# Kernel tuning notes

Measured on AMD Instinct MI355X. Metric: run time of the kernel, lower is better.

Reference implementation:

```python
import jax, jax.numpy as jnp
import numpy as np

B, P, H, D = 32, 512, 512, 512

def setup_inputs() -> dict:
    key = jax.random.key(0)
    k1, k2, k3, k4 = jax.random.split(key, 4)
    px = jax.random.normal(k1, (B, P, D), dtype=jnp.float32)
    hx = jax.random.normal(k2, (B, H, D), dtype=jnp.float32)
    p_mask = jax.random.randint(k3, (B, P), 0, 2) == 1  # True = padded
    h_mask = jax.random.randint(k4, (B, H), 0, 2) == 1
    return {"px": px, "hx": hx, "p_mask": p_mask, "h_mask": h_mask}

def reference(px, hx, p_mask, h_mask):
    # shared (unscaled) score matrix: [B, P, H]
    e = jnp.einsum('bpd,bhd->bph', px, hx)
    neg_inf = jnp.float32(-jnp.inf)
    h_bias = jnp.where(h_mask, neg_inf, 0.0).astype(e.dtype)  # [B, H]
    p_bias = jnp.where(p_mask, neg_inf, 0.0).astype(e.dtype)  # [B, P]
    # softmax over hypothesis axis -> attend px to hx
    weight_b = jax.nn.softmax(e + h_bias[:, None, :], axis=2)  # [B, P, H]
    px_hat = jnp.einsum('bph,bhd->bpd', weight_b, hx)
    # softmax over premise axis -> attend hx to px
    weight_a = jax.nn.softmax(e + p_bias[:, :, None], axis=1)  # [B, P, H]
    hx_hat = jnp.einsum('bph,bpd->bhd', weight_a, px)
    m_p = jnp.concatenate([px, px_hat, px - px_hat, px * px_hat], axis=-1)
    m_h = jnp.concatenate([hx, hx_hat, hx - hx_hat, hx * hx_hat], axis=-1)
    return (m_p, m_h)
```

## Files before the change

### kernel.cpp

```cpp
#include <hip/hip_runtime.h>
#include <math.h>

#define NB 32
#define NN 512
#define ROWC 2048ull

typedef __attribute__((ext_vector_type(8))) short bf16x8;
typedef __attribute__((ext_vector_type(4))) float f32x4;

__device__ __forceinline__ unsigned int fbits(float f) {
  union { float f; unsigned int u; } v; v.f = f; return v.u;
}
__device__ __forceinline__ float bcast(unsigned int u) {
  union { unsigned int u; float f; } v; v.u = u; return v.f;
}
__device__ __forceinline__ unsigned int bf16_rne(float f) {
  unsigned int b = fbits(f);
  return (b + 0x7FFFu + ((b >> 16) & 1u)) >> 16;
}

__device__ __forceinline__ int frag_byte(int blk, int lane, int khalf) {
  int base = ((((khalf << 3) + blk) << 6) + lane) << 4;
  int swz = (blk ^ (lane >> 4) ^ (khalf << 2)) & 7;
  return base ^ (swz << 4);
}

__global__ __launch_bounds__(256) void gemm_e_stats(
    const float* __restrict__ px, const float* __restrict__ hx,
    const int* __restrict__ p_mask, const int* __restrict__ h_mask,
    float* __restrict__ e,
    float* __restrict__ rpm, float* __restrict__ rps,
    float* __restrict__ cpm, float* __restrict__ cps) {
  __shared__ union {
    struct { char Ah[16384]; char Al[16384]; char Bh[16384]; char Bl[16384]; } s;
    float ep[64][132];
  } u;
  __shared__ int pmk[128], hmk[128];
  __shared__ float st_m[2][128], st_s[2][128], sc_m[2][128], sc_s[2][128];
  const int b = blockIdx.z;
  const float* A = px + (size_t)b * NN * NN;
  const float* B = hx + (size_t)b * NN * NN;
  float* C = e + (size_t)b * NN * NN;
  const int row0 = blockIdx.y * 128, col0 = blockIdx.x * 128;
  const int t = threadIdx.x;
  const int l = t & 63, w = t >> 6;
  const int wr = w >> 1, wc = w & 1;
  const int g = l >> 4, li = l & 15;

  if (t < 128) pmk[t] = p_mask[(size_t)b * NN + row0 + t];
  else hmk[t - 128] = h_mask[(size_t)b * NN + col0 + (t - 128)];

  f32x4 acc[4][4];
#pragma unroll
  for (int i = 0; i < 4; ++i)
#pragma unroll
    for (int j = 0; j < 4; ++j)
#pragma unroll
      for (int r = 0; r < 4; ++r) acc[i][j][r] = 0.f;

  for (int k0 = 0; k0 < NN; k0 += 64) {
    float4 fa[8], fb[8];
#pragma unroll
    for (int i = 0; i < 8; ++i) {
      int idx = i * 256 + t;
      fa[i] = *(const float4*)&A[(size_t)(row0 + (idx >> 4)) * NN + k0 + ((idx & 15) << 2)];
    }
#pragma unroll
    for (int i = 0; i < 8; ++i) {
      int idx = i * 256 + t;
      fb[i] = *(const float4*)&B[(size_t)(col0 + (idx >> 4)) * NN + k0 + ((idx & 15) << 2)];
    }
#pragma unroll
    for (int i = 0; i < 8; ++i) {
      int idx = i * 256 + t;
      int r = idx >> 4, k = (idx & 15) << 2;
      float4 f = fa[i];
      unsigned int b0 = fbits(f.x), b1 = fbits(f.y), b2 = fbits(f.z), b3 = fbits(f.w);
      unsigned int h01 = (b0 >> 16) | (b1 & 0xFFFF0000u);
      unsigned int h23 = (b2 >> 16) | (b3 & 0xFFFF0000u);
      float r0 = f.x - bcast(b0 & 0xFFFF0000u);
      float r1 = f.y - bcast(b1 & 0xFFFF0000u);
      float r2 = f.z - bcast(b2 & 0xFFFF0000u);
      float r3 = f.w - bcast(b3 & 0xFFFF0000u);
      unsigned int l01 = (fbits(r0) >> 16) | (fbits(r1) & 0xFFFF0000u);
      unsigned int l23 = (fbits(r2) >> 16) | (fbits(r3) & 0xFFFF0000u);
      int khalf = k >> 5, k8 = (k >> 3) & 3, j = k & 7;
      int byte = frag_byte(r >> 4, (r & 15) + (k8 << 4), khalf) + (j << 1);
      *(uint2*)&u.s.Ah[byte] = make_uint2(h01, h23);
      *(uint2*)&u.s.Al[byte] = make_uint2(l01, l23);
    }
#pragma unroll
    for (int i = 0; i < 8; ++i) {
      int idx = i * 256 + t;
      int r = idx >> 4, k = (idx & 15) << 2;
      float4 f = fb[i];
      unsigned int b0 = fbits(f.x), b1 = fbits(f.y), b2 = fbits(f.z), b3 = fbits(f.w);
      unsigned int h01 = (b0 >> 16) | (b1 & 0xFFFF0000u);
      unsigned int h23 = (b2 >> 16) | (b3 & 0xFFFF0000u);
      float r0 = f.x - bcast(b0 & 0xFFFF0000u);
      float r1 = f.y - bcast(b1 & 0xFFFF0000u);
      float r2 = f.z - bcast(b2 & 0xFFFF0000u);
      float r3 = f.w - bcast(b3 & 0xFFFF0000u);
      unsigned int l01 = (fbits(r0) >> 16) | (fbits(r1) & 0xFFFF0000u);
      unsigned int l23 = (fbits(r2) >> 16) | (fbits(r3) & 0xFFFF0000u);
      int khalf = k >> 5, k8 = (k >> 3) & 3, j = k & 7;
      int byte = frag_byte(r >> 4, (r & 15) + (k8 << 4), khalf) + (j << 1);
      *(uint2*)&u.s.Bh[byte] = make_uint2(h01, h23);
      *(uint2*)&u.s.Bl[byte] = make_uint2(l01, l23);
    }
    __syncthreads();
#pragma unroll
    for (int kh = 0; kh < 2; ++kh) {
      bf16x8 ah[4], al[4], bh[4], bl[4];
#pragma unroll
      for (int i = 0; i < 4; ++i) {
        int ab = frag_byte(wr * 4 + i, l, kh);
        ah[i] = *(const bf16x8*)&u.s.Ah[ab];
        al[i] = *(const bf16x8*)&u.s.Al[ab];
        int bb = frag_byte(wc * 4 + i, l, kh);
        bh[i] = *(const bf16x8*)&u.s.Bh[bb];
        bl[i] = *(const bf16x8*)&u.s.Bl[bb];
      }
#pragma unroll
      for (int i = 0; i < 4; ++i)
#pragma unroll
        for (int j = 0; j < 4; ++j) {
          acc[i][j] = __builtin_amdgcn_mfma_f32_16x16x32_bf16(ah[i], bh[j], acc[i][j], 0, 0, 0);
          acc[i][j] = __builtin_amdgcn_mfma_f32_16x16x32_bf16(ah[i], bl[j], acc[i][j], 0, 0, 0);
          acc[i][j] = __builtin_amdgcn_mfma_f32_16x16x32_bf16(al[i], bh[j], acc[i][j], 0, 0, 0);
        }
    }
    __syncthreads();
  }

#pragma unroll
  for (int i = 0; i < 4; ++i)
#pragma unroll
    for (int r = 0; r < 4; ++r) {
      float v[4];
      float m = -INFINITY;
#pragma unroll
      for (int j = 0; j < 4; ++j) {
        v[j] = hmk[wc * 64 + j * 16 + li] ? -INFINITY : acc[i][j][r];
        m = fmaxf(m, v[j]);
      }
#pragma unroll
      for (int o = 1; o < 16; o <<= 1) m = fmaxf(m, __shfl_xor(m, o));
      float s = 0.f;
#pragma unroll
      for (int j = 0; j < 4; ++j) s += (v[j] == -INFINITY) ? 0.f : __expf(v[j] - m);
#pragma unroll
      for (int o = 1; o < 16; o <<= 1) s += __shfl_xor(s, o);
      if (li == 0) {
        st_m[wc][wr * 64 + i * 16 + g * 4 + r] = m;
        st_s[wc][wr * 64 + i * 16 + g * 4 + r] = s;
      }
    }

#pragma unroll
  for (int j = 0; j < 4; ++j) {
    float v[16];
    float m = -INFINITY;
#pragma unroll
    for (int i = 0; i < 4; ++i)
#pragma unroll
      for (int r = 0; r < 4; ++r) {
        float x = pmk[wr * 64 + i * 16 + g * 4 + r] ? -INFINITY : acc[i][j][r];
        v[i * 4 + r] = x;
        m = fmaxf(m, x);
      }
    m = fmaxf(m, __shfl_xor(m, 16));
    m = fmaxf(m, __shfl_xor(m, 32));
    float s = 0.f;
#pragma unroll
    for (int q = 0; q < 16; ++q) s += (v[q] == -INFINITY) ? 0.f : __expf(v[q] - m);
    s += __shfl_xor(s, 16);
    s += __shfl_xor(s, 32);
    if (g == 0) {
      sc_m[wr][wc * 64 + j * 16 + li] = m;
      sc_s[wr][wc * 64 + j * 16 + li] = s;
    }
  }
  __syncthreads();

  if (t < 128) {
    float m0 = st_m[0][t], m1 = st_m[1][t];
    float s0 = st_s[0][t], s1 = st_s[1][t];
    float m = fmaxf(m0, m1);
    float s = 0.f;
    if (s0 > 0.f) s += s0 * __expf(m0 - m);
    if (s1 > 0.f) s += s1 * __expf(m1 - m);
    rpm[((size_t)b * 4 + blockIdx.x) * NN + row0 + t] = m;
    rps[((size_t)b * 4 + blockIdx.x) * NN + row0 + t] = s;
  } else {
    int c = t - 128;
    float m0 = sc_m[0][c], m1 = sc_m[1][c];
    float s0 = sc_s[0][c], s1 = sc_s[1][c];
    float m = fmaxf(m0, m1);
    float s = 0.f;
    if (s0 > 0.f) s += s0 * __expf(m0 - m);
    if (s1 > 0.f) s += s1 * __expf(m1 - m);
    cpm[((size_t)b * 4 + blockIdx.y) * NN + col0 + c] = m;
    cps[((size_t)b * 4 + blockIdx.y) * NN + col0 + c] = s;
  }

#pragma unroll
  for (int pass = 0; pass < 2; ++pass) {
    __syncthreads();
    if (wr == pass) {
#pragma unroll
      for (int i = 0; i < 4; ++i)
#pragma unroll
        for (int j = 0; j < 4; ++j)
#pragma unroll
          for (int r = 0; r < 4; ++r)
            u.ep[i * 16 + g * 4 + r][wc * 64 + j * 16 + li] = acc[i][j][r];
    }
    __syncthreads();
#pragma unroll
    for (int i = 0; i < 8; ++i) {
      int idx = i * 256 + t;
      int r = idx >> 5, c4 = idx & 31;
      int grow = row0 + pass * 64 + r;
      float4 v = *(const float4*)&u.ep[r][c4 * 4];
      *(float4*)&C[(size_t)grow * NN + col0 + c4 * 4] = v;
    }
  }
}

__global__ __launch_bounds__(512) void merge_stats(
    const float* __restrict__ rpm, const float* __restrict__ rps,
    const float* __restrict__ cpm, const float* __restrict__ cps,
    float* __restrict__ rmax, float* __restrict__ rinv,
    float* __restrict__ cmax, float* __restrict__ cinv) {
  const int b = blockIdx.x;
  const int t = threadIdx.x;
  const float* pm = blockIdx.y == 0 ? rpm : cpm;
  const float* ps = blockIdx.y == 0 ? rps : cps;
  float* fm = blockIdx.y == 0 ? rmax : cmax;
  float* fi = blockIdx.y == 0 ? rinv : cinv;
  float mj[4], sj[4];
  float m = -INFINITY;
#pragma unroll
  for (int j = 0; j < 4; ++j) {
    mj[j] = pm[((size_t)b * 4 + j) * NN + t];
    sj[j] = ps[((size_t)b * 4 + j) * NN + t];
    m = fmaxf(m, mj[j]);
  }
  float s = 0.f;
#pragma unroll
  for (int j = 0; j < 4; ++j)
    if (sj[j] > 0.f) s += sj[j] * __expf(mj[j] - m);
  fm[(size_t)b * NN + t] = m;
  fi[(size_t)b * NN + t] = 1.0f / s;
}

__global__ __launch_bounds__(256) void gemm_wp(
    const float* __restrict__ E, const float* __restrict__ hxg,
    const float* __restrict__ pxg, const int* __restrict__ h_mask,
    const float* __restrict__ rmax, const float* __restrict__ rinv,
    float* __restrict__ outg) {
  __shared__ union {
    struct { char A[16384]; char B[16384]; } s;
    float ep[64][132];
  } u;
  const int b = blockIdx.z;
  const float* Eb = E + (size_t)b * NN * NN;
  const float* B = hxg + (size_t)b * NN * NN;
  const float* X = pxg + (size_t)b * NN * NN;
  const int* hm = h_mask + (size_t)b * NN;
  const float* rmx = rmax + (size_t)b * NN;
  const float* rin = rinv + (size_t)b * NN;
  float* out = outg + (size_t)b * NN * ROWC;
  const int row0 = blockIdx.y * 128, col0 = blockIdx.x * 128;
  const int t = threadIdx.x;
  const int l = t & 63, w = t >> 6;
  const int wr = w >> 1, wc = w & 1;

  float rmv[8];
#pragma unroll
  for (int i = 0; i < 8; ++i) rmv[i] = rmx[row0 + ((i * 256 + t) >> 4)];

  f32x4 acc[4][4];
#pragma unroll
  for (int i = 0; i < 4; ++i)
#pragma unroll
    for (int j = 0; j < 4; ++j)
#pragma unroll
      for (int r = 0; r < 4; ++r) acc[i][j][r] = 0.f;

  for (int k0 = 0; k0 < NN; k0 += 64) {
#pragma unroll
    for (int i = 0; i < 8; ++i) {
      int idx = i * 256 + t;
      int r = idx >> 4, c4 = idx & 15, k = c4 << 2;
      float4 f = *(const float4*)&Eb[(size_t)(row0 + r) * NN + k0 + k];
      int4 m4 = *(const int4*)&hm[k0 + k];
      float w0 = m4.x ? 0.f : __expf(f.x - rmv[i]);
      float w1 = m4.y ? 0.f : __expf(f.y - rmv[i]);
      float w2 = m4.z ? 0.f : __expf(f.z - rmv[i]);
      float w3 = m4.w ? 0.f : __expf(f.w - rmv[i]);
      unsigned int p01 = bf16_rne(w0) | (bf16_rne(w1) << 16);
      unsigned int p23 = bf16_rne(w2) | (bf16_rne(w3) << 16);
      int khalf = k >> 5, k8 = (k >> 3) & 3, j = k & 7;
      int byte = frag_byte(r >> 4, (r & 15) + (k8 << 4), khalf) + (j << 1);
      *(uint2*)&u.s.A[byte] = make_uint2(p01, p23);
    }
#pragma unroll
    for (int i = 0; i < 4; ++i) {
      int idx = i * 256 + t;
      int kp = idx >> 5, nq = idx & 31;
      int k = kp << 1, n = nq << 2;
      const float* p0 = &B[(size_t)(k0 + k) * NN + col0 + n];
      float4 f0 = *(const float4*)p0;
      float4 f1 = *(const float4*)(p0 + NN);
      int khalf = k >> 5, k8 = (k >> 3) & 3, j = k & 7;
      float fa0[4] = {f0.x, f0.y, f0.z, f0.w};
      float fa1[4] = {f1.x, f1.y, f1.z, f1.w};
#pragma unroll
      for (int c = 0; c < 4; ++c) {
        unsigned int pk = bf16_rne(fa0[c]) | (bf16_rne(fa1[c]) << 16);
        int nn2 = n + c;
        int byte = frag_byte(nn2 >> 4, (nn2 & 15) + (k8 << 4), khalf) + (j << 1);
        *(unsigned int*)&u.s.B[byte] = pk;
      }
    }
    __syncthreads();
#pragma unroll
    for (int kh = 0; kh < 2; ++kh) {
      bf16x8 av[4], bv[4];
#pragma unroll
      for (int i = 0; i < 4; ++i) {
        av[i] = *(const bf16x8*)&u.s.A[frag_byte(wr * 4 + i, l, kh)];
        bv[i] = *(const bf16x8*)&u.s.B[frag_byte(wc * 4 + i, l, kh)];
      }
#pragma unroll
      for (int i = 0; i < 4; ++i)
#pragma unroll
        for (int j = 0; j < 4; ++j)
          acc[i][j] = __builtin_amdgcn_mfma_f32_16x16x32_bf16(av[i], bv[j], acc[i][j], 0, 0, 0);
    }
    __syncthreads();
  }

  const int g = l >> 4, li = l & 15;
#pragma unroll
  for (int pass = 0; pass < 2; ++pass) {
    if (wr == pass) {
#pragma unroll
      for (int i = 0; i < 4; ++i)
#pragma unroll
        for (int j = 0; j < 4; ++j)
#pragma unroll
          for (int r = 0; r < 4; ++r)
            u.ep[i * 16 + g * 4 + r][wc * 64 + j * 16 + li] = acc[i][j][r];
    }
    __syncthreads();
#pragma unroll
    for (int i = 0; i < 8; ++i) {
      int idx = i * 256 + t;
      int r = idx >> 5, c4 = idx & 31;
      int grow = row0 + pass * 64 + r;
      float ri = rin[grow];
      float4 ph = *(const float4*)&u.ep[r][c4 * 4];
      ph.x *= ri; ph.y *= ri; ph.z *= ri; ph.w *= ri;
      float4 xv = *(const float4*)&X[(size_t)grow * NN + col0 + c4 * 4];
      size_t base = (size_t)grow * ROWC + col0 + c4 * 4;
      *(float4*)&out[base] = xv;
      *(float4*)&out[base + 512] = ph;
      float4 df = {xv.x - ph.x, xv.y - ph.y, xv.z - ph.z, xv.w - ph.w};
      *(float4*)&out[base + 1024] = df;
      float4 pr = {xv.x * ph.x, xv.y * ph.y, xv.z * ph.z, xv.w * ph.w};
      *(float4*)&out[base + 1536] = pr;
    }
    __syncthreads();
  }
}

__global__ __launch_bounds__(256) void gemm_wh(
    const float* __restrict__ E, const float* __restrict__ pxg,
    const float* __restrict__ hxg, const int* __restrict__ p_mask,
    const float* __restrict__ cmax, const float* __restrict__ cinv,
    float* __restrict__ outg) {
  __shared__ union {
    struct { char A[16384]; char B[16384]; } s;
    float ep[64][132];
  } u;
  const int b = blockIdx.z;
  const float* Eb = E + (size_t)b * NN * NN;
  const float* B = pxg + (size_t)b * NN * NN;
  const float* X = hxg + (size_t)b * NN * NN;
  const int* pmsk = p_mask + (size_t)b * NN;
  const float* cmx = cmax + (size_t)b * NN;
  const float* cin = cinv + (size_t)b * NN;
  float* out = outg + (size_t)b * NN * ROWC;
  const int row0 = blockIdx.y * 128, col0 = blockIdx.x * 128;
  const int t = threadIdx.x;
  const int l = t & 63, w = t >> 6;
  const int wr = w >> 1, wc = w & 1;

  float4 cmv[4];
#pragma unroll
  for (int i = 0; i < 4; ++i) {
    int idx = i * 256 + t;
    int n = (idx & 31) << 2;
    cmv[i] = *(const float4*)&cmx[row0 + n];
  }

  f32x4 acc[4][4];
#pragma unroll
  for (int i = 0; i < 4; ++i)
#pragma unroll
    for (int j = 0; j < 4; ++j)
#pragma unroll
      for (int r = 0; r < 4; ++r) acc[i][j][r] = 0.f;

  for (int k0 = 0; k0 < NN; k0 += 64) {
#pragma unroll
    for (int i = 0; i < 4; ++i) {
      int idx = i * 256 + t;
      int kp = idx >> 5, nq = idx & 31;
      int k = kp << 1, n = nq << 2;
      const float* p0 = &Eb[(size_t)(k0 + k) * NN + row0 + n];
      float4 f0 = *(const float4*)p0;
      float4 f1 = *(const float4*)(p0 + NN);
      int pm0 = pmsk[k0 + k], pm1 = pmsk[k0 + k + 1];
      float fa0[4] = {f0.x, f0.y, f0.z, f0.w};
      float fa1[4] = {f1.x, f1.y, f1.z, f1.w};
      float cma[4] = {cmv[i].x, cmv[i].y, cmv[i].z, cmv[i].w};
      int khalf = k >> 5, k8 = (k >> 3) & 3, j = k & 7;
#pragma unroll
      for (int c = 0; c < 4; ++c) {
        float w0 = pm0 ? 0.f : __expf(fa0[c] - cma[c]);
        float w1 = pm1 ? 0.f : __expf(fa1[c] - cma[c]);
        unsigned int pk = bf16_rne(w0) | (bf16_rne(w1) << 16);
        int nn2 = n + c;
        int byte = frag_byte(nn2 >> 4, (nn2 & 15) + (k8 << 4), khalf) + (j << 1);
        *(unsigned int*)&u.s.A[byte] = pk;
      }
    }
#pragma unroll
    for (int i = 0; i < 4; ++i) {
      int idx = i * 256 + t;
      int kp = idx >> 5, nq = idx & 31;
      int k = kp << 1, n = nq << 2;
      const float* p0 = &B[(size_t)(k0 + k) * NN + col0 + n];
      float4 f0 = *(const float4*)p0;
      float4 f1 = *(const float4*)(p0 + NN);
      int khalf = k >> 5, k8 = (k >> 3) & 3, j = k & 7;
      float fa0[4] = {f0.x, f0.y, f0.z, f0.w};
      float fa1[4] = {f1.x, f1.y, f1.z, f1.w};
#pragma unroll
      for (int c = 0; c < 4; ++c) {
        unsigned int pk = bf16_rne(fa0[c]) | (bf16_rne(fa1[c]) << 16);
        int nn2 = n + c;
        int byte = frag_byte(nn2 >> 4, (nn2 & 15) + (k8 << 4), khalf) + (j << 1);
        *(unsigned int*)&u.s.B[byte] = pk;
      }
    }
    __syncthreads();
#pragma unroll
    for (int kh = 0; kh < 2; ++kh) {
      bf16x8 av[4], bv[4];
#pragma unroll
      for (int i = 0; i < 4; ++i) {
        av[i] = *(const bf16x8*)&u.s.A[frag_byte(wr * 4 + i, l, kh)];
        bv[i] = *(const bf16x8*)&u.s.B[frag_byte(wc * 4 + i, l, kh)];
      }
#pragma unroll
      for (int i = 0; i < 4; ++i)
#pragma unroll
        for (int j = 0; j < 4; ++j)
          acc[i][j] = __builtin_amdgcn_mfma_f32_16x16x32_bf16(av[i], bv[j], acc[i][j], 0, 0, 0);
    }
    __syncthreads();
  }

  const int g = l >> 4, li = l & 15;
#pragma unroll
  for (int pass = 0; pass < 2; ++pass) {
    if (wr == pass) {
#pragma unroll
      for (int i = 0; i < 4; ++i)
#pragma unroll
        for (int j = 0; j < 4; ++j)
#pragma unroll
          for (int r = 0; r < 4; ++r)
            u.ep[i * 16 + g * 4 + r][wc * 64 + j * 16 + li] = acc[i][j][r];
    }
    __syncthreads();
#pragma unroll
    for (int i = 0; i < 8; ++i) {
      int idx = i * 256 + t;
      int r = idx >> 5, c4 = idx & 31;
      int grow = row0 + pass * 64 + r;
      float ci = cin[grow];
      float4 hh = *(const float4*)&u.ep[r][c4 * 4];
      hh.x *= ci; hh.y *= ci; hh.z *= ci; hh.w *= ci;
      float4 xv = *(const float4*)&X[(size_t)grow * NN + col0 + c4 * 4];
      size_t base = (size_t)grow * ROWC + col0 + c4 * 4;
      *(float4*)&out[base] = xv;
      *(float4*)&out[base + 512] = hh;
      float4 df = {xv.x - hh.x, xv.y - hh.y, xv.z - hh.z, xv.w - hh.w};
      *(float4*)&out[base + 1024] = df;
      float4 pr = {xv.x * hh.x, xv.y * hh.y, xv.z * hh.z, xv.w * hh.w};
      *(float4*)&out[base + 1536] = pr;
    }
    __syncthreads();
  }
}

extern "C" void kernel_launch(void* const* d_in, const int* in_sizes, int n_in,
                              void* d_out, int out_size, void* d_ws, size_t ws_size,
                              hipStream_t stream) {
  const float* px = (const float*)d_in[0];
  const float* hx = (const float*)d_in[1];
  const int* p_mask = (const int*)d_in[2];
  const int* h_mask = (const int*)d_in[3];
  float* out = (float*)d_out;

  float* E = (float*)d_ws;
  float* rpm = E + (size_t)NB * NN * NN;
  float* rps = rpm + (size_t)NB * 4 * NN;
  float* cpm = rps + (size_t)NB * 4 * NN;
  float* cps = cpm + (size_t)NB * 4 * NN;
  float* rmaxv = cps + (size_t)NB * 4 * NN;
  float* rinvv = rmaxv + (size_t)NB * NN;
  float* cmaxv = rinvv + (size_t)NB * NN;
  float* cinvv = cmaxv + (size_t)NB * NN;

  dim3 blk(256);
  dim3 gg(4, 4, NB);
  gemm_e_stats<<<gg, blk, 0, stream>>>(px, hx, p_mask, h_mask, E, rpm, rps, cpm, cps);
  merge_stats<<<dim3(NB, 2), dim3(512), 0, stream>>>(rpm, rps, cpm, cps,
                                                     rmaxv, rinvv, cmaxv, cinvv);
  gemm_wp<<<gg, blk, 0, stream>>>(E, hx, px, h_mask, rmaxv, rinvv, out);
  gemm_wh<<<gg, blk, 0, stream>>>(E, px, hx, p_mask, cmaxv, cinvv,
                                  out + (size_t)NB * NN * ROWC);
}
```

Measured before the change: 228.9 us.

## Prefetch next K tile into registers and halve K-step to raise occupancy

The score GEMM kernel now uses a 32-wide K step with half-size LDS staging buffers. The next tile's global loads are issued into registers before the MFMA loop on the current tile, so memory latency overlaps with compute. The kernel also declares launch bounds of 4 blocks per CU and loads B fragments one at a time to reduce register pressure. The trade-off is twice as many barriers and loop iterations, plus tighter register limits that could cause spills.

```diff
diff --git a/kernel.cpp b/kernel.cpp
--- a/kernel.cpp
+++ b/kernel.cpp
@@ -25,14 +25,14 @@
   return base ^ (swz << 4);
 }
 
-__global__ __launch_bounds__(256) void gemm_e_stats(
+__global__ __launch_bounds__(256, 4) void gemm_e_stats(
     const float* __restrict__ px, const float* __restrict__ hx,
     const int* __restrict__ p_mask, const int* __restrict__ h_mask,
     float* __restrict__ e,
     float* __restrict__ rpm, float* __restrict__ rps,
     float* __restrict__ cpm, float* __restrict__ cps) {
   __shared__ union {
-    struct { char Ah[16384]; char Al[16384]; char Bh[16384]; char Bl[16384]; } s;
+    struct { char Ah[8192]; char Al[8192]; char Bh[8192]; char Bl[8192]; } s;
     float ep[64][132];
   } u;
   __shared__ int pmk[128], hmk[128];
@@ -58,22 +58,21 @@
 #pragma unroll
       for (int r = 0; r < 4; ++r) acc[i][j][r] = 0.f;
 
-  for (int k0 = 0; k0 < NN; k0 += 64) {
-    float4 fa[8], fb[8];
-#pragma unroll
-    for (int i = 0; i < 8; ++i) {
-      int idx = i * 256 + t;
-      fa[i] = *(const float4*)&A[(size_t)(row0 + (idx >> 4)) * NN + k0 + ((idx & 15) << 2)];
-    }
-#pragma unroll
-    for (int i = 0; i < 8; ++i) {
-      int idx = i * 256 + t;
-      fb[i] = *(const float4*)&B[(size_t)(col0 + (idx >> 4)) * NN + k0 + ((idx & 15) << 2)];
-    }
-#pragma unroll
-    for (int i = 0; i < 8; ++i) {
-      int idx = i * 256 + t;
-      int r = idx >> 4, k = (idx & 15) << 2;
+  const int srow = t >> 3, sc4 = t & 7;
+  const int sk = sc4 << 2;
+  const int sk8 = sc4 >> 1, sj = (sc4 & 1) << 2;
+  float4 fa[4], fb[4];
+#pragma unroll
+  for (int i = 0; i < 4; ++i) {
+    fa[i] = *(const float4*)&A[(size_t)(row0 + srow + 32 * i) * NN + sk];
+    fb[i] = *(const float4*)&B[(size_t)(col0 + srow + 32 * i) * NN + sk];
+  }
+
+  for (int k0 = 0; k0 < NN; k0 += 32) {
+#pragma unroll
+    for (int i = 0; i < 4; ++i) {
+      int r = srow + 32 * i;
+      int byte = frag_byte(r >> 4, (r & 15) + (sk8 << 4), 0) + (sj << 1);
       float4 f = fa[i];
       unsigned int b0 = fbits(f.x), b1 = fbits(f.y), b2 = fbits(f.z), b3 = fbits(f.w);
       unsigned int h01 = (b0 >> 16) | (b1 & 0xFFFF0000u);
@@ -84,51 +83,50 @@
       float r3 = f.w - bcast(b3 & 0xFFFF0000u);
       unsigned int l01 = (fbits(r0) >> 16) | (fbits(r1) & 0xFFFF0000u);
       unsigned int l23 = (fbits(r2) >> 16) | (fbits(r3) & 0xFFFF0000u);
-      int khalf = k >> 5, k8 = (k >> 3) & 3, j = k & 7;
-      int byte = frag_byte(r >> 4, (r & 15) + (k8 << 4), khalf) + (j << 1);
       *(uint2*)&u.s.Ah[byte] = make_uint2(h01, h23);
       *(uint2*)&u.s.Al[byte] = make_uint2(l01, l23);
-    }
-#pragma unroll
-    for (int i = 0; i < 8; ++i) {
-      int idx = i * 256 + t;
-      int r = idx >> 4, k = (idx & 15) << 2;
-      float4 f = fb[i];
-      unsigned int b0 = fbits(f.x), b1 = fbits(f.y), b2 = fbits(f.z), b3 = fbits(f.w);
-      unsigned int h01 = (b0 >> 16) | (b1 & 0xFFFF0000u);
-      unsigned int h23 = (b2 >> 16) | (b3 & 0xFFFF0000u);
-      float r0 = f.x - bcast(b0 & 0xFFFF0000u);
-      float r1 = f.y - bcast(b1 & 0xFFFF0000u);
-      float r2 = f.z - bcast(b2 & 0xFFFF0000u);
-      float r3 = f.w - bcast(b3 & 0xFFFF0000u);
-      unsigned int l01 = (fbits(r0) >> 16) | (fbits(r1) & 0xFFFF0000u);
-      unsigned int l23 = (fbits(r2) >> 16) | (fbits(r3) & 0xFFFF0000u);
-      int khalf = k >> 5, k8 = (k >> 3) & 3, j = k & 7;
-      int byte = frag_byte(r >> 4, (r & 15) + (k8 << 4), khalf) + (j << 1);
+      f = fb[i];
+      b0 = fbits(f.x); b1 = fbits(f.y); b2 = fbits(f.z); b3 = fbits(f.w);
+      h01 = (b0 >> 16) | (b1 & 0xFFFF0000u);
+      h23 = (b2 >> 16) | (b3 & 0xFFFF0000u);
+      r0 = f.x - bcast(b0 & 0xFFFF0000u);
+      r1 = f.y - bcast(b1 & 0xFFFF0000u);
+      r2 = f.z - bcast(b2 & 0xFFFF0000u);
+      r3 = f.w - bcast(b3 & 0xFFFF0000u);
+      l01 = (fbits(r0) >> 16) | (fbits(r1) & 0xFFFF0000u);
+      l23 = (fbits(r2) >> 16) | (fbits(r3) & 0xFFFF0000u);
       *(uint2*)&u.s.Bh[byte] = make_uint2(h01, h23);
       *(uint2*)&u.s.Bl[byte] = make_uint2(l01, l23);
     }
     __syncthreads();
-#pragma unroll
-    for (int kh = 0; kh < 2; ++kh) {
-      bf16x8 ah[4], al[4], bh[4], bl[4];
+
+    bf16x8 ah[4], al[4];
+#pragma unroll
+    for (int i = 0; i < 4; ++i) {
+      int ab = frag_byte(wr * 4 + i, l, 0);
+      ah[i] = *(const bf16x8*)&u.s.Ah[ab];
+      al[i] = *(const bf16x8*)&u.s.Al[ab];
+    }
+
+    if (k0 + 32 < NN) {
 #pragma unroll
       for (int i = 0; i < 4; ++i) {
-        int ab = frag_byte(wr * 4 + i, l, kh);
-        ah[i] = *(const bf16x8*)&u.s.Ah[ab];
-        al[i] = *(const bf16x8*)&u.s.Al[ab];
-        int bb = frag_byte(wc * 4 + i, l, kh);
-        bh[i] = *(const bf16x8*)&u.s.Bh[bb];
-        bl[i] = *(const bf16x8*)&u.s.Bl[bb];
-      }
-#pragma unroll
-      for (int i = 0; i < 4; ++i)
-#pragma unroll
-        for (int j = 0; j < 4; ++j) {
-          acc[i][j] = __builtin_amdgcn_mfma_f32_16x16x32_bf16(ah[i], bh[j], acc[i][j], 0, 0, 0);
-          acc[i][j] = __builtin_amdgcn_mfma_f32_16x16x32_bf16(ah[i], bl[j], acc[i][j], 0, 0, 0);
-          acc[i][j] = __builtin_amdgcn_mfma_f32_16x16x32_bf16(al[i], bh[j], acc[i][j], 0, 0, 0);
-        }
+        fa[i] = *(const float4*)&A[(size_t)(row0 + srow + 32 * i) * NN + k0 + 32 + sk];
+        fb[i] = *(const float4*)&B[(size_t)(col0 + srow + 32 * i) * NN + k0 + 32 + sk];
+      }
+    }
+
+#pragma unroll
+    for (int j = 0; j < 4; ++j) {
+      int bb = frag_byte(wc * 4 + j, l, 0);
+      bf16x8 bh = *(const bf16x8*)&u.s.Bh[bb];
+      bf16x8 bl = *(const bf16x8*)&u.s.Bl[bb];
+#pragma unroll
+      for (int i = 0; i < 4; ++i) {
+        acc[i][j] = __builtin_amdgcn_mfma_f32_16x16x32_bf16(ah[i], bh, acc[i][j], 0, 0, 0);
+        acc[i][j] = __builtin_amdgcn_mfma_f32_16x16x32_bf16(ah[i], bl, acc[i][j], 0, 0, 0);
+        acc[i][j] = __builtin_amdgcn_mfma_f32_16x16x32_bf16(al[i], bh, acc[i][j], 0, 0, 0);
+      }
     }
     __syncthreads();
   }
```

Result: slower. 283.3 us (+23.8%).

## Use 512 threads in score GEMM to halve per-wave tile and registers

Applied to the files above, without the earlier changes.

The first GEMM kernel (scores plus softmax partial stats) moves from 256 to 512 threads per block, so each wave owns a 32x64 output sub-tile instead of 64x64. The accumulator array and A fragments shrink, B fragments are loaded one at a time inside the MFMA loop, and global loads are interleaved with the bf16 split instead of staged in registers first. Column stats now merge four wave-row partials instead of two. The goal is lower register pressure and more waves to hide latency. The cost is more LDS fragment reads per MFMA, and the global-load prefetch that batched all loads up front is gone.

```diff
diff --git a/kernel.cpp b/kernel.cpp
--- a/kernel.cpp
+++ b/kernel.cpp
@@ -25,7 +25,7 @@
   return base ^ (swz << 4);
 }
 
-__global__ __launch_bounds__(256) void gemm_e_stats(
+__global__ __launch_bounds__(512) void gemm_e_stats(
     const float* __restrict__ px, const float* __restrict__ hx,
     const int* __restrict__ p_mask, const int* __restrict__ h_mask,
     float* __restrict__ e,
@@ -36,7 +36,7 @@
     float ep[64][132];
   } u;
   __shared__ int pmk[128], hmk[128];
-  __shared__ float st_m[2][128], st_s[2][128], sc_m[2][128], sc_s[2][128];
+  __shared__ float st_m[2][128], st_s[2][128], sc_m[4][128], sc_s[4][128];
   const int b = blockIdx.z;
   const float* A = px + (size_t)b * NN * NN;
   const float* B = hx + (size_t)b * NN * NN;
@@ -48,33 +48,24 @@
   const int g = l >> 4, li = l & 15;
 
   if (t < 128) pmk[t] = p_mask[(size_t)b * NN + row0 + t];
-  else hmk[t - 128] = h_mask[(size_t)b * NN + col0 + (t - 128)];
-
-  f32x4 acc[4][4];
-#pragma unroll
-  for (int i = 0; i < 4; ++i)
+  else if (t < 256) hmk[t - 128] = h_mask[(size_t)b * NN + col0 + (t - 128)];
+
+  f32x4 acc[2][4];
+#pragma unroll
+  for (int i = 0; i < 2; ++i)
 #pragma unroll
     for (int j = 0; j < 4; ++j)
 #pragma unroll
       for (int r = 0; r < 4; ++r) acc[i][j][r] = 0.f;
 
   for (int k0 = 0; k0 < NN; k0 += 64) {
-    float4 fa[8], fb[8];
-#pragma unroll
-    for (int i = 0; i < 8; ++i) {
-      int idx = i * 256 + t;
-      fa[i] = *(const float4*)&A[(size_t)(row0 + (idx >> 4)) * NN + k0 + ((idx & 15) << 2)];
-    }
-#pragma unroll
-    for (int i = 0; i < 8; ++i) {
-      int idx = i * 256 + t;
-      fb[i] = *(const float4*)&B[(size_t)(col0 + (idx >> 4)) * NN + k0 + ((idx & 15) << 2)];
-    }
-#pragma unroll
-    for (int i = 0; i < 8; ++i) {
-      int idx = i * 256 + t;
-      int r = idx >> 4, k = (idx & 15) << 2;
-      float4 f = fa[i];
+#pragma unroll
+    for (int i = 0; i < 4; ++i) {
+      int idx = i * 512 + t;
+      int r = idx >> 4, c4 = idx & 15, k = c4 << 2;
+      int khalf = k >> 5, k8 = (k >> 3) & 3, j = k & 7;
+      int byte = frag_byte(r >> 4, (r & 15) + (k8 << 4), khalf) + (j << 1);
+      float4 f = *(const float4*)&A[(size_t)(row0 + r) * NN + k0 + k];
       unsigned int b0 = fbits(f.x), b1 = fbits(f.y), b2 = fbits(f.z), b3 = fbits(f.w);
       unsigned int h01 = (b0 >> 16) | (b1 & 0xFFFF0000u);
       unsigned int h23 = (b2 >> 16) | (b3 & 0xFFFF0000u);
@@ -84,16 +75,16 @@
       float r3 = f.w - bcast(b3 & 0xFFFF0000u);
       unsigned int l01 = (fbits(r0) >> 16) | (fbits(r1) & 0xFFFF0000u);
       unsigned int l23 = (fbits(r2) >> 16) | (fbits(r3) & 0xFFFF0000u);
+      *(uint2*)&u.s.Ah[byte] = make_uint2(h01, h23);
+      *(uint2*)&u.s.Al[byte] = make_uint2(l01, l23);
+    }
+#pragma unroll
+    for (int i = 0; i < 4; ++i) {
+      int idx = i * 512 + t;
+      int r = idx >> 4, c4 = idx & 15, k = c4 << 2;
       int khalf = k >> 5, k8 = (k >> 3) & 3, j = k & 7;
       int byte = frag_byte(r >> 4, (r & 15) + (k8 << 4), khalf) + (j << 1);
-      *(uint2*)&u.s.Ah[byte] = make_uint2(h01, h23);
-      *(uint2*)&u.s.Al[byte] = make_uint2(l01, l23);
-    }
-#pragma unroll
-    for (int i = 0; i < 8; ++i) {
-      int idx = i * 256 + t;
-      int r = idx >> 4, k = (idx & 15) << 2;
-      float4 f = fb[i];
+      float4 f = *(const float4*)&B[(size_t)(col0 + r) * NN + k0 + k];
       unsigned int b0 = fbits(f.x), b1 = fbits(f.y), b2 = fbits(f.z), b3 = fbits(f.w);
       unsigned int h01 = (b0 >> 16) | (b1 & 0xFFFF0000u);
       unsigned int h23 = (b2 >> 16) | (b3 & 0xFFFF0000u);
@@ -103,38 +94,38 @@
       float r3 = f.w - bcast(b3 & 0xFFFF0000u);
       unsigned int l01 = (fbits(r0) >> 16) | (fbits(r1) & 0xFFFF0000u);
       unsigned int l23 = (fbits(r2) >> 16) | (fbits(r3) & 0xFFFF0000u);
-      int khalf = k >> 5, k8 = (k >> 3) & 3, j = k & 7;
-      int byte = frag_byte(r >> 4, (r & 15) + (k8 << 4), khalf) + (j << 1);
       *(uint2*)&u.s.Bh[byte] = make_uint2(h01, h23);
       *(uint2*)&u.s.Bl[byte] = make_uint2(l01, l23);
     }
     __syncthreads();
+
 #pragma unroll
     for (int kh = 0; kh < 2; ++kh) {
-      bf16x8 ah[4], al[4], bh[4], bl[4];
-#pragma unroll
-      for (int i = 0; i < 4; ++i) {
-        int ab = frag_byte(wr * 4 + i, l, kh);
+      bf16x8 ah[2], al[2];
+#pragma unroll
+      for (int i = 0; i < 2; ++i) {
+        int ab = frag_byte(wr * 2 + i, l, kh);
         ah[i] = *(const bf16x8*)&u.s.Ah[ab];
         al[i] = *(const bf16x8*)&u.s.Al[ab];
-        int bb = frag_byte(wc * 4 + i, l, kh);
-        bh[i] = *(const bf16x8*)&u.s.Bh[bb];
-        bl[i] = *(const bf16x8*)&u.s.Bl[bb];
-      }
-#pragma unroll
-      for (int i = 0; i < 4; ++i)
-#pragma unroll
-        for (int j = 0; j < 4; ++j) {
-          acc[i][j] = __builtin_amdgcn_mfma_f32_16x16x32_bf16(ah[i], bh[j], acc[i][j], 0, 0, 0);
-          acc[i][j] = __builtin_amdgcn_mfma_f32_16x16x32_bf16(ah[i], bl[j], acc[i][j], 0, 0, 0);
-          acc[i][j] = __builtin_amdgcn_mfma_f32_16x16x32_bf16(al[i], bh[j], acc[i][j], 0, 0, 0);
+      }
+#pragma unroll
+      for (int j = 0; j < 4; ++j) {
+        int bb = frag_byte(wc * 4 + j, l, kh);
+        bf16x8 bh = *(const bf16x8*)&u.s.Bh[bb];
+        bf16x8 bl = *(const bf16x8*)&u.s.Bl[bb];
+#pragma unroll
+        for (int i = 0; i < 2; ++i) {
+          acc[i][j] = __builtin_amdgcn_mfma_f32_16x16x32_bf16(ah[i], bh, acc[i][j], 0, 0, 0);
+          acc[i][j] = __builtin_amdgcn_mfma_f32_16x16x32_bf16(ah[i], bl, acc[i][j], 0, 0, 0);
+          acc[i][j] = __builtin_amdgcn_mfma_f32_16x16x32_bf16(al[i], bh, acc[i][j], 0, 0, 0);
         }
-    }
-    __syncthreads();
-  }
-
-#pragma unroll
-  for (int i = 0; i < 4; ++i)
+      }
+    }
+    __syncthreads();
+  }
+
+#pragma unroll
+  for (int i = 0; i < 2; ++i)
 #pragma unroll
     for (int r = 0; r < 4; ++r) {
       float v[4];
@@ -152,20 +143,20 @@
 #pragma unroll
       for (int o = 1; o < 16; o <<= 1) s += __shfl_xor(s, o);
       if (li == 0) {
-        st_m[wc][wr * 64 + i * 16 + g * 4 + r] = m;
-        st_s[wc][wr * 64 + i * 16 + g * 4 + r] = s;
+        st_m[wc][wr * 32 + i * 16 + g * 4 + r] = m;
+        st_s[wc][wr * 32 + i * 16 + g * 4 + r] = s;
       }
     }
 
 #pragma unroll
   for (int j = 0; j < 4; ++j) {
-    float v[16];
+    float v[8];
     float m = -INFINITY;
 #pragma unroll
-    for (int i = 0; i < 4; ++i)
+    for (int i = 0; i < 2; ++i)
 #pragma unroll
       for (int r = 0; r < 4; ++r) {
-        float x = pmk[wr * 64 + i * 16 + g * 4 + r] ? -INFINITY : acc[i][j][r];
+        float x = pmk[wr * 32 + i * 16 + g * 4 + r] ? -INFINITY : acc[i][j][r];
         v[i * 4 + r] = x;
         m = fmaxf(m, x);
       }
@@ -173,7 +164,7 @@
     m = fmaxf(m, __shfl_xor(m, 32));
     float s = 0.f;
 #pragma unroll
-    for (int q = 0; q < 16; ++q) s += (v[q] == -INFINITY) ? 0.f : __expf(v[q] - m);
+    for (int q = 0; q < 8; ++q) s += (v[q] == -INFINITY) ? 0.f : __expf(v[q] - m);
     s += __shfl_xor(s, 16);
     s += __shfl_xor(s, 32);
     if (g == 0) {
@@ -192,14 +183,15 @@
     if (s1 > 0.f) s += s1 * __expf(m1 - m);
     rpm[((size_t)b * 4 + blockIdx.x) * NN + row0 + t] = m;
     rps[((size_t)b * 4 + blockIdx.x) * NN + row0 + t] = s;
-  } else {
+  } else if (t < 256) {
     int c = t - 128;
-    float m0 = sc_m[0][c], m1 = sc_m[1][c];
-    float s0 = sc_s[0][c], s1 = sc_s[1][c];
-    float m = fmaxf(m0, m1);
+    float m = sc_m[0][c];
+#pragma unroll
+    for (int q = 1; q < 4; ++q) m = fmaxf(m, sc_m[q][c]);
     float s = 0.f;
-    if (s0 > 0.f) s += s0 * __expf(m0 - m);
-    if (s1 > 0.f) s += s1 * __expf(m1 - m);
+#pragma unroll
+    for (int q = 0; q < 4; ++q)
+      if (sc_s[q][c] > 0.f) s += sc_s[q][c] * __expf(sc_m[q][c] - m);
     cpm[((size_t)b * 4 + blockIdx.y) * NN + col0 + c] = m;
     cps[((size_t)b * 4 + blockIdx.y) * NN + col0 + c] = s;
   }
@@ -207,19 +199,19 @@
 #pragma unroll
   for (int pass = 0; pass < 2; ++pass) {
     __syncthreads();
-    if (wr == pass) {
-#pragma unroll
-      for (int i = 0; i < 4; ++i)
+    if ((wr >> 1) == pass) {
+#pragma unroll
+      for (int i = 0; i < 2; ++i)
 #pragma unroll
         for (int j = 0; j < 4; ++j)
 #pragma unroll
           for (int r = 0; r < 4; ++r)
-            u.ep[i * 16 + g * 4 + r][wc * 64 + j * 16 + li] = acc[i][j][r];
-    }
-    __syncthreads();
-#pragma unroll
-    for (int i = 0; i < 8; ++i) {
-      int idx = i * 256 + t;
+            u.ep[(wr & 1) * 32 + i * 16 + g * 4 + r][wc * 64 + j * 16 + li] = acc[i][j][r];
+    }
+    __syncthreads();
+#pragma unroll
+    for (int i = 0; i < 4; ++i) {
+      int idx = i * 512 + t;
       int r = idx >> 5, c4 = idx & 31;
       int grow = row0 + pass * 64 + r;
       float4 v = *(const float4*)&u.ep[r][c4 * 4];
@@ -529,12 +521,11 @@
   float* cmaxv = rinvv + (size_t)NB * NN;
   float* cinvv = cmaxv + (size_t)NB * NN;
 
-  dim3 blk(256);
   dim3 gg(4, 4, NB);
-  gemm_e_stats<<<gg, blk, 0, stream>>>(px, hx, p_mask, h_mask, E, rpm, rps, cpm, cps);
+  gemm_e_stats<<<gg, dim3(512), 0, stream>>>(px, hx, p_mask, h_mask, E, rpm, rps, cpm, cps);
   merge_stats<<<dim3(NB, 2), dim3(512), 0, stream>>>(rpm, rps, cpm, cps,
                                                      rmaxv, rinvv, cmaxv, cinvv);
-  gemm_wp<<<gg, blk, 0, stream>>>(E, hx, px, h_mask, rmaxv, rinvv, out);
-  gemm_wh<<<gg, blk, 0, stream>>>(E, px, hx, p_mask, cmaxv, cinvv,
-                                  out + (size_t)NB * NN * ROWC);
-}
+  gemm_wp<<<gg, dim3(256), 0, stream>>>(E, hx, px, h_mask, rmaxv, rinvv, out);
+  gemm_wh<<<gg, dim3(256), 0, stream>>>(E, px, hx, p_mask, cmaxv, cinvv,
+                                        out + (size_t)NB * NN * ROWC);
+}
```

Result: slower. 250.0 us (+9.3%).

## Pre-split px/hx into tiled bf16 hi/lo buffers in a separate conversion kernel

Applied to the files above, without the earlier changes.

Adds a convert_tiled kernel that splits px and hx once into bf16 high and low parts, stored in an MFMA-fragment-ready tiled layout in workspace. gemm_e_stats then copies these pre-arranged tiles straight into LDS instead of loading fp32 and converting and swizzling per tile. Each A tile was previously converted 4 times (once per column block), and likewise for B, so this removes redundant conversion ALU work and the scattered LDS stores. The cost is an extra kernel launch plus a write and reread of 4 bf16 buffers, and the LDS layout loses its swizzle, which may cause bank conflicts.

```diff
diff --git a/kernel.cpp b/kernel.cpp
--- a/kernel.cpp
+++ b/kernel.cpp
@@ -25,21 +25,54 @@
   return base ^ (swz << 4);
 }
 
+__global__ __launch_bounds__(256) void convert_tiled(
+    const float* __restrict__ px, const float* __restrict__ hx,
+    uint4* __restrict__ pxh, uint4* __restrict__ pxl,
+    uint4* __restrict__ hxh, uint4* __restrict__ hxl) {
+  const int bp = blockIdx.x;
+  const float* src = (blockIdx.y ? hx : px) + (size_t)bp * 128 * NN;
+  uint4* dh = (blockIdx.y ? hxh : pxh) + (size_t)bp * 16 * 512;
+  uint4* dl = (blockIdx.y ? hxl : pxl) + (size_t)bp * 16 * 512;
+  const int t = threadIdx.x;
+#pragma unroll
+  for (int i = 0; i < 8; ++i) {
+    int idx = i * 256 + t;
+    int ks = idx >> 7, row = idx & 127;
+    const float* rp = src + (size_t)row * NN + ks * 32;
+    int ub = ks * 512 + (row >> 4) * 64 + (row & 15);
+#pragma unroll
+    for (int ko = 0; ko < 4; ++ko) {
+      float4 f0 = *(const float4*)(rp + ko * 8);
+      float4 f1 = *(const float4*)(rp + ko * 8 + 4);
+      float ff[8] = {f0.x, f0.y, f0.z, f0.w, f1.x, f1.y, f1.z, f1.w};
+      union { unsigned short us[8]; uint4 u4; } hi, lo;
+#pragma unroll
+      for (int q = 0; q < 8; ++q) {
+        unsigned int bq = fbits(ff[q]);
+        hi.us[q] = (unsigned short)(bq >> 16);
+        float r = ff[q] - bcast(bq & 0xFFFF0000u);
+        lo.us[q] = (unsigned short)(fbits(r) >> 16);
+      }
+      dh[ub + 16 * ko] = hi.u4;
+      dl[ub + 16 * ko] = lo.u4;
+    }
+  }
+}
+
 __global__ __launch_bounds__(256) void gemm_e_stats(
-    const float* __restrict__ px, const float* __restrict__ hx,
+    const uint4* __restrict__ Ahg, const uint4* __restrict__ Alg,
+    const uint4* __restrict__ Bhg, const uint4* __restrict__ Blg,
     const int* __restrict__ p_mask, const int* __restrict__ h_mask,
     float* __restrict__ e,
     float* __restrict__ rpm, float* __restrict__ rps,
     float* __restrict__ cpm, float* __restrict__ cps) {
   __shared__ union {
-    struct { char Ah[16384]; char Al[16384]; char Bh[16384]; char Bl[16384]; } s;
+    struct { uint4 Ah[512]; uint4 Al[512]; uint4 Bh[512]; uint4 Bl[512]; } s;
     float ep[64][132];
   } u;
   __shared__ int pmk[128], hmk[128];
   __shared__ float st_m[2][128], st_s[2][128], sc_m[2][128], sc_s[2][128];
   const int b = blockIdx.z;
-  const float* A = px + (size_t)b * NN * NN;
-  const float* B = hx + (size_t)b * NN * NN;
   float* C = e + (size_t)b * NN * NN;
   const int row0 = blockIdx.y * 128, col0 = blockIdx.x * 128;
   const int t = threadIdx.x;
@@ -50,6 +83,11 @@
   if (t < 128) pmk[t] = p_mask[(size_t)b * NN + row0 + t];
   else hmk[t - 128] = h_mask[(size_t)b * NN + col0 + (t - 128)];
 
+  const uint4* gAh = Ahg + ((size_t)(b * 4 + blockIdx.y) * 16) * 512;
+  const uint4* gAl = Alg + ((size_t)(b * 4 + blockIdx.y) * 16) * 512;
+  const uint4* gBh = Bhg + ((size_t)(b * 4 + blockIdx.x) * 16) * 512;
+  const uint4* gBl = Blg + ((size_t)(b * 4 + blockIdx.x) * 16) * 512;
+
   f32x4 acc[4][4];
 #pragma unroll
   for (int i = 0; i < 4; ++i)
@@ -58,77 +96,52 @@
 #pragma unroll
       for (int r = 0; r < 4; ++r) acc[i][j][r] = 0.f;
 
-  for (int k0 = 0; k0 < NN; k0 += 64) {
-    float4 fa[8], fb[8];
-#pragma unroll
-    for (int i = 0; i < 8; ++i) {
-      int idx = i * 256 + t;
-      fa[i] = *(const float4*)&A[(size_t)(row0 + (idx >> 4)) * NN + k0 + ((idx & 15) << 2)];
-    }
-#pragma unroll
-    for (int i = 0; i < 8; ++i) {
-      int idx = i * 256 + t;
-      fb[i] = *(const float4*)&B[(size_t)(col0 + (idx >> 4)) * NN + k0 + ((idx & 15) << 2)];
-    }
-#pragma unroll
-    for (int i = 0; i < 8; ++i) {
-      int idx = i * 256 + t;
-      int r = idx >> 4, k = (idx & 15) << 2;
-      float4 f = fa[i];
-      unsigned int b0 = fbits(f.x), b1 = fbits(f.y), b2 = fbits(f.z), b3 = fbits(f.w);
-      unsigned int h01 = (b0 >> 16) | (b1 & 0xFFFF0000u);
-      unsigned int h23 = (b2 >> 16) | (b3 & 0xFFFF0000u);
-      float r0 = f.x - bcast(b0 & 0xFFFF0000u);
-      float r1 = f.y - bcast(b1 & 0xFFFF0000u);
-      float r2 = f.z - bcast(b2 & 0xFFFF0000u);
-      float r3 = f.w - bcast(b3 & 0xFFFF0000u);
-      unsigned int l01 = (fbits(r0) >> 16) | (fbits(r1) & 0xFFFF0000u);
-      unsigned int l23 = (fbits(r2) >> 16) | (fbits(r3) & 0xFFFF0000u);
-      int khalf = k >> 5, k8 = (k >> 3) & 3, j = k & 7;
-      int byte = frag_byte(r >> 4, (r & 15) + (k8 << 4), khalf) + (j << 1);
-      *(uint2*)&u.s.Ah[byte] = make_uint2(h01, h23);
-      *(uint2*)&u.s.Al[byte] = make_uint2(l01, l23);
-    }
-#pragma unroll
-    for (int i = 0; i < 8; ++i) {
-      int idx = i * 256 + t;
-      int r = idx >> 4, k = (idx & 15) << 2;
-      float4 f = fb[i];
-      unsigned int b0 = fbits(f.x), b1 = fbits(f.y), b2 = fbits(f.z), b3 = fbits(f.w);
-      unsigned int h01 = (b0 >> 16) | (b1 & 0xFFFF0000u);
-      unsigned int h23 = (b2 >> 16) | (b3 & 0xFFFF0000u);
-      float r0 = f.x - bcast(b0 & 0xFFFF0000u);
-      float r1 = f.y - bcast(b1 & 0xFFFF0000u);
-      float r2 = f.z - bcast(b2 & 0xFFFF0000u);
-      float r3 = f.w - bcast(b3 & 0xFFFF0000u);
-      unsigned int l01 = (fbits(r0) >> 16) | (fbits(r1) & 0xFFFF0000u);
-      unsigned int l23 = (fbits(r2) >> 16) | (fbits(r3) & 0xFFFF0000u);
-      int khalf = k >> 5, k8 = (k >> 3) & 3, j = k & 7;
-      int byte = frag_byte(r >> 4, (r & 15) + (k8 << 4), khalf) + (j << 1);
-      *(uint2*)&u.s.Bh[byte] = make_uint2(h01, h23);
-      *(uint2*)&u.s.Bl[byte] = make_uint2(l01, l23);
-    }
-    __syncthreads();
-#pragma unroll
-    for (int kh = 0; kh < 2; ++kh) {
-      bf16x8 ah[4], al[4], bh[4], bl[4];
+  for (int ks = 0; ks < 16; ++ks) {
+    const int o = ks * 512;
+    u.s.Ah[t] = gAh[o + t];        u.s.Ah[t + 256] = gAh[o + t + 256];
+    u.s.Al[t] = gAl[o + t];        u.s.Al[t + 256] = gAl[o + t + 256];
+    u.s.Bh[t] = gBh[o + t];        u.s.Bh[t + 256] = gBh[o + t + 256];
+    u.s.Bl[t] = gBl[o + t];        u.s.Bl[t + 256] = gBl[o + t + 256];
+    __syncthreads();
+
+    {
+      bf16x8 fa[4], fb[4];
 #pragma unroll
       for (int i = 0; i < 4; ++i) {
-        int ab = frag_byte(wr * 4 + i, l, kh);
-        ah[i] = *(const bf16x8*)&u.s.Ah[ab];
-        al[i] = *(const bf16x8*)&u.s.Al[ab];
-        int bb = frag_byte(wc * 4 + i, l, kh);
-        bh[i] = *(const bf16x8*)&u.s.Bh[bb];
-        bl[i] = *(const bf16x8*)&u.s.Bl[bb];
-      }
-#pragma unroll
-      for (int i = 0; i < 4; ++i)
-#pragma unroll
-        for (int j = 0; j < 4; ++j) {
-          acc[i][j] = __builtin_amdgcn_mfma_f32_16x16x32_bf16(ah[i], bh[j], acc[i][j], 0, 0, 0);
-          acc[i][j] = __builtin_amdgcn_mfma_f32_16x16x32_bf16(ah[i], bl[j], acc[i][j], 0, 0, 0);
-          acc[i][j] = __builtin_amdgcn_mfma_f32_16x16x32_bf16(al[i], bh[j], acc[i][j], 0, 0, 0);
-        }
+        fa[i] = *(const bf16x8*)&u.s.Al[(wr * 4 + i) * 64 + l];
+        fb[i] = *(const bf16x8*)&u.s.Bh[(wc * 4 + i) * 64 + l];
+      }
+#pragma unroll
+      for (int i = 0; i < 4; ++i)
+#pragma unroll
+        for (int j = 0; j < 4; ++j)
+          acc[i][j] = __builtin_amdgcn_mfma_f32_16x16x32_bf16(fa[i], fb[j], acc[i][j], 0, 0, 0);
+    }
+    {
+      bf16x8 fa[4], fb[4];
+#pragma unroll
+      for (int i = 0; i < 4; ++i) {
+        fa[i] = *(const bf16x8*)&u.s.Ah[(wr * 4 + i) * 64 + l];
+        fb[i] = *(const bf16x8*)&u.s.Bl[(wc * 4 + i) * 64 + l];
+      }
+#pragma unroll
+      for (int i = 0; i < 4; ++i)
+#pragma unroll
+        for (int j = 0; j < 4; ++j)
+          acc[i][j] = __builtin_amdgcn_mfma_f32_16x16x32_bf16(fa[i], fb[j], acc[i][j], 0, 0, 0);
+    }
+    {
+      bf16x8 fa[4], fb[4];
+#pragma unroll
+      for (int i = 0; i < 4; ++i) {
+        fa[i] = *(const bf16x8*)&u.s.Ah[(wr * 4 + i) * 64 + l];
+        fb[i] = *(const bf16x8*)&u.s.Bh[(wc * 4 + i) * 64 + l];
+      }
+#pragma unroll
+      for (int i = 0; i < 4; ++i)
+#pragma unroll
+        for (int j = 0; j < 4; ++j)
+          acc[i][j] = __builtin_amdgcn_mfma_f32_16x16x32_bf16(fa[i], fb[j], acc[i][j], 0, 0, 0);
     }
     __syncthreads();
   }
@@ -519,8 +532,14 @@
   const int* h_mask = (const int*)d_in[3];
   float* out = (float*)d_out;
 
+  const size_t NE = (size_t)NB * NN * NN;
+  const size_t NU = (size_t)NB * 4 * 16 * 512;
   float* E = (float*)d_ws;
-  float* rpm = E + (size_t)NB * NN * NN;
+  uint4* pxh = (uint4*)(E + NE);
+  uint4* pxl = pxh + NU;
+  uint4* hxh = pxl + NU;
+  uint4* hxl = hxh + NU;
+  float* rpm = (float*)(hxl + NU);
   float* rps = rpm + (size_t)NB * 4 * NN;
   float* cpm = rps + (size_t)NB * 4 * NN;
   float* cps = cpm + (size_t)NB * 4 * NN;
@@ -529,12 +548,13 @@
   float* cmaxv = rinvv + (size_t)NB * NN;
   float* cinvv = cmaxv + (size_t)NB * NN;
 
-  dim3 blk(256);
   dim3 gg(4, 4, NB);
-  gemm_e_stats<<<gg, blk, 0, stream>>>(px, hx, p_mask, h_mask, E, rpm, rps, cpm, cps);
+  convert_tiled<<<dim3(128, 2), dim3(256), 0, stream>>>(px, hx, pxh, pxl, hxh, hxl);
+  gemm_e_stats<<<gg, dim3(256), 0, stream>>>(pxh, pxl, hxh, hxl, p_mask, h_mask,
+                                             E, rpm, rps, cpm, cps);
   merge_stats<<<dim3(NB, 2), dim3(512), 0, stream>>>(rpm, rps, cpm, cps,
                                                      rmaxv, rinvv, cmaxv, cinvv);
-  gemm_wp<<<gg, blk, 0, stream>>>(E, hx, px, h_mask, rmaxv, rinvv, out);
-  gemm_wh<<<gg, blk, 0, stream>>>(E, px, hx, p_mask, cmaxv, cinvv,
-                                  out + (size_t)NB * NN * ROWC);
-}
+  gemm_wp<<<gg, dim3(256), 0, stream>>>(E, hx, px, h_mask, rmaxv, rinvv, out);
+  gemm_wh<<<gg, dim3(256), 0, stream>>>(E, px, hx, p_mask, cmaxv, cinvv,
+                                        out + (size_t)NB * NN * ROWC);
+}
```

Result: faster. 208.4 us (-8.9%).
